# Performance work log

Measured on AMD Instinct MI355X. Metric: run time of the kernel, lower is better.

## Reference

```python
import jax, jax.numpy as jnp
import numpy as np

D_MODEL = 512
D_STATE = 64
L_SEQ = 4096
BATCH = 4


def _make_A(N):
    # HiPPO-LegS style A: A[n,k] = -sqrt(2n+1)sqrt(2k+1) if n>k, -(n+1) if n==k, 0 else (n,k from 1..N)
    idx = np.arange(1, N + 1, dtype=np.float64)
    M = np.sqrt(2 * idx[:, None] + 1) * np.sqrt(2 * idx[None, :] + 1)
    lower = (idx[:, None] > idx[None, :]).astype(np.float64)
    return -(lower * M + np.diag(idx + 1))


def _discretize(A, B, C, step):
    # bilinear (Tustin) transform
    I = np.eye(A.shape[0])
    BL = np.linalg.inv(I - step / 2.0 * A)
    Ab = BL @ (I + step / 2.0 * A)
    Bb = (BL * step) @ B
    return Ab, Bb, C


def setup_inputs() -> dict:
    key = jax.random.key(0)
    rng = np.random.RandomState(0)
    A = _make_A(D_STATE)
    B = rng.randn(D_STATE, 1)
    C = rng.randn(1, D_STATE)
    Ab, Bb, Cb = _discretize(A, B, C, step=1.0 / L_SEQ)
    u = jax.random.normal(key, (BATCH, L_SEQ, D_MODEL), dtype=jnp.float32)
    return {
        "u": u,
        "A_": jnp.asarray(Ab, dtype=jnp.float32),
        "B_": jnp.asarray(Bb, dtype=jnp.float32),
        "C_": jnp.asarray(Cb, dtype=jnp.float32),
    }


def reference(u, A_, B_, C_):
    # u: (B, L, D) -> flatten channels: (BD, L)
    b, L, d = u.shape
    uc = u.transpose(0, 2, 1).reshape(b * d, L)
    N = A_.shape[0]
    b_vec = B_[:, 0]  # (N,)
    c_vec = C_[0]     # (N,)

    def step(x, u_k):
        # x: (BD, N), u_k: (BD,)
        # x_k = A_ @ x_{k-1}^T + B_ @ u_k^T  (expressed batched as x @ A_.T + outer)
        x_new = x @ A_.T + u_k[:, None] * b_vec[None, :]
        y_k = x_new @ c_vec  # (BD,)
        return x_new, y_k

    x0 = jnp.zeros((b * d, N), dtype=u.dtype)
    _, ys = jax.lax.scan(step, x0, uc.T)  # ys: (L, BD)
    y = ys.T.reshape(b, d, L).transpose(0, 2, 1)  # (B, L, D)
    return y
```

## Files before the change

kernel.cpp:

```cpp
#include <hip/hip_runtime.h>

#define L_SEQ   4096
#define D_MODEL 512
#define NSEQ    2048
#define CH      128
#define NC      32

#define OFF_P    0
#define OFF_W1T  4096
#define OFF_WOUT 12288
#define OFF_KLOC 20480
#define OFF_GX   20736

#define BC(v, j) __int_as_float(__builtin_amdgcn_readlane(__float_as_int(v), (j)))

__global__ __launch_bounds__(256) void k_prep(
    const float* __restrict__ A, const float* __restrict__ B,
    const float* __restrict__ C, float* __restrict__ ws) {
  __shared__ float Srow[64][68];
  __shared__ float STs[64][68];
  __shared__ float vrT[128][68];
  __shared__ float cwS[129][68];
  __shared__ float Cs[64], Bsh[64];

  const int tid = threadIdx.x;
  if (tid < 64) { Cs[tid] = C[tid]; Bsh[tid] = B[tid]; }
  for (int e = tid; e < 4096; e += 256) {
    const float a = A[e];
    Srow[e >> 6][e & 63] = a;
    STs[e & 63][e >> 6] = a;
  }
  __syncthreads();

  if (tid < 64) {
    vrT[0][tid] = Bsh[tid];
    float acc = 0.f;
#pragma unroll
    for (int k = 0; k < 64; ++k) acc += Cs[k] * STs[tid][k];
    cwS[1][tid] = acc;
  }
  __syncthreads();

  const int iy4 = (tid >> 4) * 4, jx4 = (tid & 15) * 4;

  for (int t = 0; t < 7; ++t) {
    const int nd = 1 << t;

    if (nd <= 2) {
      const int total = 2 * nd * 64;
      if (tid < total) {
        const int half = (tid >= nd * 64);
        const int o = (tid >> 6) & (nd - 1);
        const int idx = tid & 63;
        float acc = 0.f;
        if (!half) {
#pragma unroll
          for (int k = 0; k < 64; ++k) acc += vrT[o][k] * Srow[idx][k];
          vrT[nd + o][idx] = acc;
        } else {
#pragma unroll
          for (int k = 0; k < 64; ++k) acc += cwS[1 + o][k] * STs[idx][k];
          cwS[nd + 1 + o][idx] = acc;
        }
      }
    } else {
      const int tilesPerGemm = nd * 4;
      for (int tt = tid; tt < 2 * tilesPerGemm; tt += 256) {
        const int half = (tt >= tilesPerGemm);
        const int q = half ? tt - tilesPerGemm : tt;
        const int m0 = (q >> 4) * 4;
        const int i0 = (q & 15) * 4;
        float acc[4][4] = {{0.f}};
        if (!half) {
#pragma unroll 4
          for (int k = 0; k < 64; k += 4) {
            float a_[4][4];
#pragma unroll
            for (int r = 0; r < 4; ++r)
              *(float4*)&a_[r][0] = *(const float4*)&vrT[m0 + r][k];
#pragma unroll
            for (int kk = 0; kk < 4; ++kk) {
              const float4 b4 = *(const float4*)&STs[k + kk][i0];
#pragma unroll
              for (int r = 0; r < 4; ++r) {
                const float av = a_[r][kk];
                acc[r][0] += av * b4.x; acc[r][1] += av * b4.y;
                acc[r][2] += av * b4.z; acc[r][3] += av * b4.w;
              }
            }
          }
#pragma unroll
          for (int r = 0; r < 4; ++r) {
            float4 v; v.x = acc[r][0]; v.y = acc[r][1]; v.z = acc[r][2]; v.w = acc[r][3];
            *(float4*)&vrT[nd + m0 + r][i0] = v;
          }
        } else {
#pragma unroll 4
          for (int k = 0; k < 64; k += 4) {
            float a_[4][4];
#pragma unroll
            for (int r = 0; r < 4; ++r)
              *(float4*)&a_[r][0] = *(const float4*)&cwS[1 + m0 + r][k];
#pragma unroll
            for (int kk = 0; kk < 4; ++kk) {
              const float4 b4 = *(const float4*)&Srow[k + kk][i0];
#pragma unroll
              for (int r = 0; r < 4; ++r) {
                const float av = a_[r][kk];
                acc[r][0] += av * b4.x; acc[r][1] += av * b4.y;
                acc[r][2] += av * b4.z; acc[r][3] += av * b4.w;
              }
            }
          }
#pragma unroll
          for (int r = 0; r < 4; ++r) {
            float4 v; v.x = acc[r][0]; v.y = acc[r][1]; v.z = acc[r][2]; v.w = acc[r][3];
            *(float4*)&cwS[nd + 1 + m0 + r][i0] = v;
          }
        }
      }
    }

    float sacc[4][4] = {{0.f}};
#pragma unroll 4
    for (int k = 0; k < 64; k += 4) {
      float a_[4][4];
#pragma unroll
      for (int r = 0; r < 4; ++r)
        *(float4*)&a_[r][0] = *(const float4*)&Srow[iy4 + r][k];
#pragma unroll
      for (int kk = 0; kk < 4; ++kk) {
        const float4 b4 = *(const float4*)&Srow[k + kk][jx4];
#pragma unroll
        for (int r = 0; r < 4; ++r) {
          const float av = a_[r][kk];
          sacc[r][0] += av * b4.x; sacc[r][1] += av * b4.y;
          sacc[r][2] += av * b4.z; sacc[r][3] += av * b4.w;
        }
      }
    }
    __syncthreads();
#pragma unroll
    for (int r = 0; r < 4; ++r) {
      float4 v; v.x = sacc[r][0]; v.y = sacc[r][1]; v.z = sacc[r][2]; v.w = sacc[r][3];
      *(float4*)&Srow[iy4 + r][jx4] = v;
    }
#pragma unroll
    for (int c = 0; c < 4; ++c) {
      float4 v; v.x = sacc[0][c]; v.y = sacc[1][c]; v.z = sacc[2][c]; v.w = sacc[3][c];
      *(float4*)&STs[jx4 + c][iy4] = v;
    }
    __syncthreads();
  }

  float* Pg = ws + OFF_P;
  for (int e = tid; e < 4096; e += 256) Pg[e] = Srow[e >> 6][e & 63];

  float* W1Tg = ws + OFF_W1T;
  for (int e = tid; e < 8192; e += 256) W1Tg[e] = vrT[127 - (e >> 6)][e & 63];

  float* Wg = ws + OFF_WOUT;
  for (int e = tid; e < 8192; e += 256) Wg[e] = cwS[(e & 127) + 1][e >> 7];

  float* Kz = ws + OFF_KLOC;
  if (tid < 128) {
    float acc = 0.f;
#pragma unroll
    for (int i = 0; i < 64; ++i) acc += Cs[i] * vrT[tid][i];
    Kz[128 + tid] = acc;
  } else {
    Kz[tid - 128] = 0.f;
  }
}

__global__ __launch_bounds__(256) void k_proj(
    const float* __restrict__ u, const float* __restrict__ wsr,
    float* __restrict__ gx) {
  __shared__ float W1s[128][66];
  __shared__ float Us[64][132];

  const int st = blockIdx.x;
  const int c = blockIdx.y;
  const int tid = threadIdx.x;
  const int sgl = st * 128;
  const int bi = sgl >> 9, d0 = sgl & 511;

  const float* W1Tg = wsr + OFF_W1T;
#pragma unroll
  for (int k = 0; k < 32; ++k) {
    const int e = tid + 256 * k;
    W1s[e >> 6][e & 63] = W1Tg[e];
  }

  const float* ub = u + ((size_t)bi * L_SEQ + c * CH) * D_MODEL + d0;
  const int sy4 = (tid >> 3) * 4;
  const int ix8 = (tid & 7) * 8;

  float acc[4][8];
#pragma unroll
  for (int r = 0; r < 4; ++r)
#pragma unroll
    for (int cc = 0; cc < 8; ++cc) acc[r][cc] = 0.f;

  for (int h = 0; h < 2; ++h) {
    __syncthreads();
#pragma unroll
    for (int e8 = 0; e8 < 8; ++e8) {
      const int e = tid + 256 * e8;
      const int rr = e >> 5, s4 = (e & 31) * 4;
      *(float4*)&Us[rr][s4] =
          *(const float4*)(ub + (size_t)(h * 64 + rr) * D_MODEL + s4);
    }
    __syncthreads();
#pragma unroll 4
    for (int rr = 0; rr < 64; ++rr) {
      const int r = h * 64 + rr;
      const float4 a = *(const float4*)&Us[rr][sy4];
      const float4 b0 = *(const float4*)&W1s[r][ix8];
      const float4 b1 = *(const float4*)&W1s[r][ix8 + 4];
      acc[0][0] += a.x * b0.x; acc[0][1] += a.x * b0.y; acc[0][2] += a.x * b0.z; acc[0][3] += a.x * b0.w;
      acc[0][4] += a.x * b1.x; acc[0][5] += a.x * b1.y; acc[0][6] += a.x * b1.z; acc[0][7] += a.x * b1.w;
      acc[1][0] += a.y * b0.x; acc[1][1] += a.y * b0.y; acc[1][2] += a.y * b0.z; acc[1][3] += a.y * b0.w;
      acc[1][4] += a.y * b1.x; acc[1][5] += a.y * b1.y; acc[1][6] += a.y * b1.z; acc[1][7] += a.y * b1.w;
      acc[2][0] += a.z * b0.x; acc[2][1] += a.z * b0.y; acc[2][2] += a.z * b0.z; acc[2][3] += a.z * b0.w;
      acc[2][4] += a.z * b1.x; acc[2][5] += a.z * b1.y; acc[2][6] += a.z * b1.z; acc[2][7] += a.z * b1.w;
      acc[3][0] += a.w * b0.x; acc[3][1] += a.w * b0.y; acc[3][2] += a.w * b0.z; acc[3][3] += a.w * b0.w;
      acc[3][4] += a.w * b1.x; acc[3][5] += a.w * b1.y; acc[3][6] += a.w * b1.z; acc[3][7] += a.w * b1.w;
    }
  }

  float* gb = gx + ((size_t)c * NSEQ + sgl) * 64;
#pragma unroll
  for (int as = 0; as < 4; ++as) {
    float4 v0, v1;
    v0.x = acc[as][0]; v0.y = acc[as][1]; v0.z = acc[as][2]; v0.w = acc[as][3];
    v1.x = acc[as][4]; v1.y = acc[as][5]; v1.z = acc[as][6]; v1.w = acc[as][7];
    float* row = gb + (size_t)(sy4 + as) * 64 + ix8;
    *(float4*)row = v0;
    *(float4*)(row + 4) = v1;
  }
}

__global__ __launch_bounds__(256) void k_scan(
    const float* __restrict__ wsr, float* __restrict__ gx) {
  const int lane = threadIdx.x & 63, wv = threadIdx.x >> 6;
  const int s = blockIdx.x * 4 + wv;

  float p[64];
  {
    const float* pr = wsr + OFF_P + lane * 64;
#pragma unroll
    for (int j = 0; j < 64; j += 4) {
      const float4 v = *(const float4*)(pr + j);
      p[j] = v.x; p[j + 1] = v.y; p[j + 2] = v.z; p[j + 3] = v.w;
    }
  }

  const size_t CS = (size_t)NSEQ * 64;
  float* gs = gx + (size_t)s * 64 + lane;
  float x = 0.f;
  float g0 = gs[0];
  float g1 = gs[CS];
  float g2 = gs[2 * CS];
  for (int c = 0; c < NC; ++c) {
    const float gn = (c + 3 < NC) ? gs[(size_t)(c + 3) * CS] : 0.f;
    gs[(size_t)c * CS] = x;
    float x0 = g0, x1 = 0.f;
#pragma unroll
    for (int j = 0; j < 64; j += 2) {
      x0 += p[j] * BC(x, j);
      x1 += p[j + 1] * BC(x, j + 1);
    }
    x = x0 + x1;
    g0 = g1; g1 = g2; g2 = gn;
  }
}

__global__ __launch_bounds__(256) void k_localout(
    const float* __restrict__ u, const float* __restrict__ wsr,
    const float* __restrict__ gx, float* __restrict__ out) {
  __shared__ float As[64][68];
  __shared__ float Bs[64][132];

  const int sg = blockIdx.x;
  const int tr = blockIdx.y;
  const int c = tr >> 1, par = tr & 1;
  const int r0 = par * 64;
  const int sgl = sg * 128;
  const int bi = sgl >> 9, d0 = sgl & 511;

  const float* KlocZ = wsr + OFF_KLOC;
  const float* WoutG = wsr + OFF_WOUT;
  const float* ub = u + ((size_t)bi * L_SEQ + c * CH) * D_MODEL + d0;

  const int tid = threadIdx.x;
  const int ty4 = (tid >> 4) * 4;
  const int tx8 = (tid & 15) * 8;

  float acc[4][8];
#pragma unroll
  for (int r = 0; r < 4; ++r)
#pragma unroll
    for (int cc = 0; cc < 8; ++cc) acc[r][cc] = 0.f;

  for (int kt = 0; kt <= par; ++kt) {
    const int k0 = kt * 64;
#pragma unroll
    for (int e8 = 0; e8 < 8; ++e8) {
      const int e = tid + 256 * e8;
      const int kk = e >> 5, s4 = (e & 31) * 4;
      *(float4*)&Bs[kk][s4] = *(const float4*)(ub + (size_t)(k0 + kk) * D_MODEL + s4);
    }
    const int base = 128 + r0 - k0;
#pragma unroll
    for (int e4 = 0; e4 < 16; ++e4) {
      const int e = tid + 256 * e4;
      const int kk = e >> 6, i = e & 63;
      As[kk][i] = KlocZ[base + i - kk];
    }
    __syncthreads();
#pragma unroll 4
    for (int kk = 0; kk < 64; ++kk) {
      const float4 a = *(const float4*)&As[kk][ty4];
      const float4 b0 = *(const float4*)&Bs[kk][tx8];
      const float4 b1 = *(const float4*)&Bs[kk][tx8 + 4];
      acc[0][0] += a.x * b0.x; acc[0][1] += a.x * b0.y; acc[0][2] += a.x * b0.z; acc[0][3] += a.x * b0.w;
      acc[0][4] += a.x * b1.x; acc[0][5] += a.x * b1.y; acc[0][6] += a.x * b1.z; acc[0][7] += a.x * b1.w;
      acc[1][0] += a.y * b0.x; acc[1][1] += a.y * b0.y; acc[1][2] += a.y * b0.z; acc[1][3] += a.y * b0.w;
      acc[1][4] += a.y * b1.x; acc[1][5] += a.y * b1.y; acc[1][6] += a.y * b1.z; acc[1][7] += a.y * b1.w;
      acc[2][0] += a.z * b0.x; acc[2][1] += a.z * b0.y; acc[2][2] += a.z * b0.z; acc[2][3] += a.z * b0.w;
      acc[2][4] += a.z * b1.x; acc[2][5] += a.z * b1.y; acc[2][6] += a.z * b1.z; acc[2][7] += a.z * b1.w;
      acc[3][0] += a.w * b0.x; acc[3][1] += a.w * b0.y; acc[3][2] += a.w * b0.z; acc[3][3] += a.w * b0.w;
      acc[3][4] += a.w * b1.x; acc[3][5] += a.w * b1.y; acc[3][6] += a.w * b1.z; acc[3][7] += a.w * b1.w;
    }
    __syncthreads();
  }

  {
    const float* xc = gx + ((size_t)c * NSEQ + sgl) * 64;
#pragma unroll
    for (int e8 = 0; e8 < 8; ++e8) {
      const int e = tid + 256 * e8;
      const int sl = e >> 4, i4 = (e & 15) * 4;
      const float4 v = *(const float4*)(xc + (size_t)sl * 64 + i4);
      Bs[i4 + 0][sl] = v.x;
      Bs[i4 + 1][sl] = v.y;
      Bs[i4 + 2][sl] = v.z;
      Bs[i4 + 3][sl] = v.w;
    }
#pragma unroll
    for (int e4 = 0; e4 < 16; ++e4) {
      const int e = tid + 256 * e4;
      const int i_ = e >> 6, r = e & 63;
      As[i_][r] = WoutG[i_ * 128 + r0 + r];
    }
    __syncthreads();
#pragma unroll 4
    for (int kk = 0; kk < 64; ++kk) {
      const float4 a = *(const float4*)&As[kk][ty4];
      const float4 b0 = *(const float4*)&Bs[kk][tx8];
      const float4 b1 = *(const float4*)&Bs[kk][tx8 + 4];
      acc[0][0] += a.x * b0.x; acc[0][1] += a.x * b0.y; acc[0][2] += a.x * b0.z; acc[0][3] += a.x * b0.w;
      acc[0][4] += a.x * b1.x; acc[0][5] += a.x * b1.y; acc[0][6] += a.x * b1.z; acc[0][7] += a.x * b1.w;
      acc[1][0] += a.y * b0.x; acc[1][1] += a.y * b0.y; acc[1][2] += a.y * b0.z; acc[1][3] += a.y * b0.w;
      acc[1][4] += a.y * b1.x; acc[1][5] += a.y * b1.y; acc[1][6] += a.y * b1.z; acc[1][7] += a.y * b1.w;
      acc[2][0] += a.z * b0.x; acc[2][1] += a.z * b0.y; acc[2][2] += a.z * b0.z; acc[2][3] += a.z * b0.w;
      acc[2][4] += a.z * b1.x; acc[2][5] += a.z * b1.y; acc[2][6] += a.z * b1.z; acc[2][7] += a.z * b1.w;
      acc[3][0] += a.w * b0.x; acc[3][1] += a.w * b0.y; acc[3][2] += a.w * b0.z; acc[3][3] += a.w * b0.w;
      acc[3][4] += a.w * b1.x; acc[3][5] += a.w * b1.y; acc[3][6] += a.w * b1.z; acc[3][7] += a.w * b1.w;
    }
  }

  float* ob = out + ((size_t)bi * L_SEQ + c * CH + r0) * D_MODEL + d0;
#pragma unroll
  for (int r = 0; r < 4; ++r) {
    float4 v0, v1;
    v0.x = acc[r][0]; v0.y = acc[r][1]; v0.z = acc[r][2]; v0.w = acc[r][3];
    v1.x = acc[r][4]; v1.y = acc[r][5]; v1.z = acc[r][6]; v1.w = acc[r][7];
    float* row = ob + (size_t)(ty4 + r) * D_MODEL + tx8;
    *(float4*)row = v0;
    *(float4*)(row + 4) = v1;
  }
}

extern "C" void kernel_launch(void* const* d_in, const int* in_sizes, int n_in,
                              void* d_out, int out_size, void* d_ws,
                              size_t ws_size, hipStream_t stream) {
  const float* u = (const float*)d_in[0];
  const float* A = (const float*)d_in[1];
  const float* B = (const float*)d_in[2];
  const float* C = (const float*)d_in[3];
  float* out = (float*)d_out;
  float* ws = (float*)d_ws;
  float* gx = ws + OFF_GX;

  k_prep<<<1, 256, 0, stream>>>(A, B, C, ws);
  k_proj<<<dim3(16, 32), 256, 0, stream>>>(u, ws, gx);
  k_scan<<<512, 256, 0, stream>>>(ws, gx);
  k_localout<<<dim3(16, 64), 256, 0, stream>>>(u, ws, gx, out);
}
```

Before: 199.8 us.

## Merge row-half blocks in k_localout into 128x128 tiles with 8x8 register blocking

k_localout now handles a full 128-row chunk per block instead of splitting it into two 64-row halves, so the u and gx tiles are loaded once per chunk rather than twice. Each thread computes an 8x8 output micro-tile with double-buffered shared-memory register prefetch, and the Wout load is vectorised. The grid halves to 512 blocks, and the upper-triangle half now runs both k-tiles, including the zero part of the Toeplitz kernel that was previously skipped. This raises register pressure and lowers block count.

```diff
diff --git a/kernel.cpp b/kernel.cpp
--- a/kernel.cpp
+++ b/kernel.cpp
@@ -279,13 +279,11 @@
 __global__ __launch_bounds__(256) void k_localout(
     const float* __restrict__ u, const float* __restrict__ wsr,
     const float* __restrict__ gx, float* __restrict__ out) {
-  __shared__ float As[64][68];
+  __shared__ float As[64][132];
   __shared__ float Bs[64][132];
 
   const int sg = blockIdx.x;
-  const int tr = blockIdx.y;
-  const int c = tr >> 1, par = tr & 1;
-  const int r0 = par * 64;
+  const int c = blockIdx.y;
   const int sgl = sg * 128;
   const int bi = sgl >> 9, d0 = sgl & 511;
 
@@ -294,16 +292,17 @@
   const float* ub = u + ((size_t)bi * L_SEQ + c * CH) * D_MODEL + d0;
 
   const int tid = threadIdx.x;
-  const int ty4 = (tid >> 4) * 4;
-  const int tx8 = (tid & 15) * 8;
-
-  float acc[4][8];
-#pragma unroll
-  for (int r = 0; r < 4; ++r)
+  const int lane = tid & 63, w = tid >> 6;
+  const int ry8 = (w * 4 + (lane >> 4)) * 8;
+  const int sx4 = (lane & 15) * 4;
+
+  float acc[8][8];
+#pragma unroll
+  for (int r = 0; r < 8; ++r)
 #pragma unroll
     for (int cc = 0; cc < 8; ++cc) acc[r][cc] = 0.f;
 
-  for (int kt = 0; kt <= par; ++kt) {
+  for (int kt = 0; kt < 2; ++kt) {
     const int k0 = kt * 64;
 #pragma unroll
     for (int e8 = 0; e8 < 8; ++e8) {
@@ -311,27 +310,36 @@
       const int kk = e >> 5, s4 = (e & 31) * 4;
       *(float4*)&Bs[kk][s4] = *(const float4*)(ub + (size_t)(k0 + kk) * D_MODEL + s4);
     }
-    const int base = 128 + r0 - k0;
-#pragma unroll
-    for (int e4 = 0; e4 < 16; ++e4) {
+    const int base = 128 - k0;
+#pragma unroll
+    for (int e4 = 0; e4 < 32; ++e4) {
       const int e = tid + 256 * e4;
-      const int kk = e >> 6, i = e & 63;
-      As[kk][i] = KlocZ[base + i - kk];
-    }
-    __syncthreads();
-#pragma unroll 4
-    for (int kk = 0; kk < 64; ++kk) {
-      const float4 a = *(const float4*)&As[kk][ty4];
-      const float4 b0 = *(const float4*)&Bs[kk][tx8];
-      const float4 b1 = *(const float4*)&Bs[kk][tx8 + 4];
-      acc[0][0] += a.x * b0.x; acc[0][1] += a.x * b0.y; acc[0][2] += a.x * b0.z; acc[0][3] += a.x * b0.w;
-      acc[0][4] += a.x * b1.x; acc[0][5] += a.x * b1.y; acc[0][6] += a.x * b1.z; acc[0][7] += a.x * b1.w;
-      acc[1][0] += a.y * b0.x; acc[1][1] += a.y * b0.y; acc[1][2] += a.y * b0.z; acc[1][3] += a.y * b0.w;
-      acc[1][4] += a.y * b1.x; acc[1][5] += a.y * b1.y; acc[1][6] += a.y * b1.z; acc[1][7] += a.y * b1.w;
-      acc[2][0] += a.z * b0.x; acc[2][1] += a.z * b0.y; acc[2][2] += a.z * b0.z; acc[2][3] += a.z * b0.w;
-      acc[2][4] += a.z * b1.x; acc[2][5] += a.z * b1.y; acc[2][6] += a.z * b1.z; acc[2][7] += a.z * b1.w;
-      acc[3][0] += a.w * b0.x; acc[3][1] += a.w * b0.y; acc[3][2] += a.w * b0.z; acc[3][3] += a.w * b0.w;
-      acc[3][4] += a.w * b1.x; acc[3][5] += a.w * b1.y; acc[3][6] += a.w * b1.z; acc[3][7] += a.w * b1.w;
+      const int kk = e >> 7, r = e & 127;
+      As[kk][r] = KlocZ[base + r - kk];
+    }
+    __syncthreads();
+    {
+      float4 a0 = *(const float4*)&As[0][ry8];
+      float4 a1 = *(const float4*)&As[0][ry8 + 4];
+      float4 b0 = *(const float4*)&Bs[0][sx4];
+      float4 b1 = *(const float4*)&Bs[0][64 + sx4];
+#pragma unroll 8
+      for (int kk = 0; kk < 64; ++kk) {
+        float4 na0 = a0, na1 = a1, nb0 = b0, nb1 = b1;
+        if (kk < 63) {
+          na0 = *(const float4*)&As[kk + 1][ry8];
+          na1 = *(const float4*)&As[kk + 1][ry8 + 4];
+          nb0 = *(const float4*)&Bs[kk + 1][sx4];
+          nb1 = *(const float4*)&Bs[kk + 1][64 + sx4];
+        }
+        const float av[8] = {a0.x, a0.y, a0.z, a0.w, a1.x, a1.y, a1.z, a1.w};
+        const float bv[8] = {b0.x, b0.y, b0.z, b0.w, b1.x, b1.y, b1.z, b1.w};
+#pragma unroll
+        for (int ii = 0; ii < 8; ++ii)
+#pragma unroll
+          for (int jj = 0; jj < 8; ++jj) acc[ii][jj] += av[ii] * bv[jj];
+        a0 = na0; a1 = na1; b0 = nb0; b1 = nb1;
+      }
     }
     __syncthreads();
   }
@@ -349,37 +357,46 @@
       Bs[i4 + 3][sl] = v.w;
     }
 #pragma unroll
-    for (int e4 = 0; e4 < 16; ++e4) {
+    for (int e4 = 0; e4 < 8; ++e4) {
       const int e = tid + 256 * e4;
-      const int i_ = e >> 6, r = e & 63;
-      As[i_][r] = WoutG[i_ * 128 + r0 + r];
-    }
-    __syncthreads();
-#pragma unroll 4
-    for (int kk = 0; kk < 64; ++kk) {
-      const float4 a = *(const float4*)&As[kk][ty4];
-      const float4 b0 = *(const float4*)&Bs[kk][tx8];
-      const float4 b1 = *(const float4*)&Bs[kk][tx8 + 4];
-      acc[0][0] += a.x * b0.x; acc[0][1] += a.x * b0.y; acc[0][2] += a.x * b0.z; acc[0][3] += a.x * b0.w;
-      acc[0][4] += a.x * b1.x; acc[0][5] += a.x * b1.y; acc[0][6] += a.x * b1.z; acc[0][7] += a.x * b1.w;
-      acc[1][0] += a.y * b0.x; acc[1][1] += a.y * b0.y; acc[1][2] += a.y * b0.z; acc[1][3] += a.y * b0.w;
-      acc[1][4] += a.y * b1.x; acc[1][5] += a.y * b1.y; acc[1][6] += a.y * b1.z; acc[1][7] += a.y * b1.w;
-      acc[2][0] += a.z * b0.x; acc[2][1] += a.z * b0.y; acc[2][2] += a.z * b0.z; acc[2][3] += a.z * b0.w;
-      acc[2][4] += a.z * b1.x; acc[2][5] += a.z * b1.y; acc[2][6] += a.z * b1.z; acc[2][7] += a.z * b1.w;
-      acc[3][0] += a.w * b0.x; acc[3][1] += a.w * b0.y; acc[3][2] += a.w * b0.z; acc[3][3] += a.w * b0.w;
-      acc[3][4] += a.w * b1.x; acc[3][5] += a.w * b1.y; acc[3][6] += a.w * b1.z; acc[3][7] += a.w * b1.w;
-    }
-  }
-
-  float* ob = out + ((size_t)bi * L_SEQ + c * CH + r0) * D_MODEL + d0;
-#pragma unroll
-  for (int r = 0; r < 4; ++r) {
+      const int i_ = e >> 5, r4 = (e & 31) * 4;
+      *(float4*)&As[i_][r4] = *(const float4*)(WoutG + i_ * 128 + r4);
+    }
+    __syncthreads();
+    {
+      float4 a0 = *(const float4*)&As[0][ry8];
+      float4 a1 = *(const float4*)&As[0][ry8 + 4];
+      float4 b0 = *(const float4*)&Bs[0][sx4];
+      float4 b1 = *(const float4*)&Bs[0][64 + sx4];
+#pragma unroll 8
+      for (int kk = 0; kk < 64; ++kk) {
+        float4 na0 = a0, na1 = a1, nb0 = b0, nb1 = b1;
+        if (kk < 63) {
+          na0 = *(const float4*)&As[kk + 1][ry8];
+          na1 = *(const float4*)&As[kk + 1][ry8 + 4];
+          nb0 = *(const float4*)&Bs[kk + 1][sx4];
+          nb1 = *(const float4*)&Bs[kk + 1][64 + sx4];
+        }
+        const float av[8] = {a0.x, a0.y, a0.z, a0.w, a1.x, a1.y, a1.z, a1.w};
+        const float bv[8] = {b0.x, b0.y, b0.z, b0.w, b1.x, b1.y, b1.z, b1.w};
+#pragma unroll
+        for (int ii = 0; ii < 8; ++ii)
+#pragma unroll
+          for (int jj = 0; jj < 8; ++jj) acc[ii][jj] += av[ii] * bv[jj];
+        a0 = na0; a1 = na1; b0 = nb0; b1 = nb1;
+      }
+    }
+  }
+
+  float* ob = out + ((size_t)bi * L_SEQ + c * CH) * D_MODEL + d0;
+#pragma unroll
+  for (int r = 0; r < 8; ++r) {
     float4 v0, v1;
     v0.x = acc[r][0]; v0.y = acc[r][1]; v0.z = acc[r][2]; v0.w = acc[r][3];
     v1.x = acc[r][4]; v1.y = acc[r][5]; v1.z = acc[r][6]; v1.w = acc[r][7];
-    float* row = ob + (size_t)(ty4 + r) * D_MODEL + tx8;
-    *(float4*)row = v0;
-    *(float4*)(row + 4) = v1;
+    float* row = ob + (size_t)(ry8 + r) * D_MODEL;
+    *(float4*)(row + sx4) = v0;
+    *(float4*)(row + 64 + sx4) = v1;
   }
 }
 
@@ -397,5 +414,5 @@
   k_prep<<<1, 256, 0, stream>>>(A, B, C, ws);
   k_proj<<<dim3(16, 32), 256, 0, stream>>>(u, ws, gx);
   k_scan<<<512, 256, 0, stream>>>(ws, gx);
-  k_localout<<<dim3(16, 64), 256, 0, stream>>>(u, ws, gx, out);
+  k_localout<<<dim3(16, 32), 256, 0, stream>>>(u, ws, gx, out);
 }
```

Result: slower. 219.6 us (+9.9%).
